# Optimization experiments

Hardware: AMD Instinct MI355X
Metric: run time of the kernel (lower is better)

## Reference

```python
import jax, jax.numpy as jnp
import numpy as np

B, L, D = 64, 1, 1024
H, HD = 16, 64          # num_heads, head_dim
T = 2048                # max kv-cache length
DFF = 4 * D
EPS = 1e-5


def _layernorm(x, w, b):
    mu = jnp.mean(x, axis=-1, keepdims=True)
    var = jnp.mean(jnp.square(x - mu), axis=-1, keepdims=True)
    return (x - mu) * jax.lax.rsqrt(var + EPS) * w + b


def setup_inputs() -> dict:
    key = jax.random.key(0)
    ks = jax.random.split(key, 12)
    s = 0.02
    x = jax.random.normal(ks[0], (B, L, D), jnp.float32)
    k_cache = jax.random.normal(ks[1], (B, H, T, HD), jnp.float32)
    v_cache = jax.random.normal(ks[2], (B, H, T, HD), jnp.float32)
    kv_cache_len = jax.random.randint(ks[3], (B,), 1024, T - 1)
    batch_indices = jnp.arange(B)
    # attend to all cache slots up to and including the newly written token
    attn_mask = (jnp.arange(T)[None, None, None, :] <= kv_cache_len[:, None, None, None])
    return {
        "x": x, "k_cache": k_cache, "v_cache": v_cache,
        "attn_mask": attn_mask, "kv_cache_len": kv_cache_len,
        "batch_indices": batch_indices,
        "qkv_w": jax.random.normal(ks[4], (D, 3 * D), jnp.float32) * s,
        "qkv_b": jnp.zeros((3 * D,), jnp.float32),
        "out_w": jax.random.normal(ks[5], (D, D), jnp.float32) * s,
        "out_b": jnp.zeros((D,), jnp.float32),
        "ln1_w": jnp.ones((D,), jnp.float32), "ln1_b": jnp.zeros((D,), jnp.float32),
        "ln2_w": jnp.ones((D,), jnp.float32), "ln2_b": jnp.zeros((D,), jnp.float32),
        "mlp_w1": jax.random.normal(ks[6], (D, DFF), jnp.float32) * s,
        "mlp_b1": jnp.zeros((DFF,), jnp.float32),
        "mlp_w2": jax.random.normal(ks[7], (DFF, D), jnp.float32) * s,
        "mlp_b2": jnp.zeros((D,), jnp.float32),
    }


def reference(x, k_cache, v_cache, attn_mask, kv_cache_len, batch_indices,
              qkv_w, qkv_b, out_w, out_b, ln1_w, ln1_b, ln2_w, ln2_b,
              mlp_w1, mlp_b1, mlp_w2, mlp_b2):
    b, l, d = x.shape
    residual = x
    qkv = (x @ qkv_w + qkv_b).reshape(b, l, 3, H, HD)
    q, k, v = qkv[:, :, 0], qkv[:, :, 1], qkv[:, :, 2]   # [B,L,H,HD]
    q = jnp.transpose(q, (0, 2, 1, 3))                    # [B,H,1,HD]
    k = jnp.transpose(k, (0, 2, 1, 3))
    v = jnp.transpose(v, (0, 2, 1, 3))
    # scatter new K/V into per-batch cache slot kv_cache_len
    k_cache = k_cache.at[batch_indices, :, kv_cache_len].set(k[:, :, 0])
    v_cache = v_cache.at[batch_indices, :, kv_cache_len].set(v[:, :, 0])
    # SDPA over full cache, single query token
    scores = jnp.einsum("bhqd,bhkd->bhqk", q, k_cache) * (1.0 / np.sqrt(HD))
    scores = jnp.where(attn_mask, scores, -jnp.inf)       # bool mask: True = attend
    attn = jax.nn.softmax(scores, axis=-1)
    o = jnp.einsum("bhqk,bhkd->bhqd", attn, v_cache)
    o = jnp.transpose(o, (0, 2, 1, 3)).reshape(b, l, d)
    x = residual + (o @ out_w + out_b)
    x = _layernorm(x, ln1_w, ln1_b)
    residual = x
    h = jax.nn.relu(x @ mlp_w1 + mlp_b1) @ mlp_w2 + mlp_b2
    x = _layernorm(residual + h, ln2_w, ln2_b)
    return x
```

## Files before the change

### kernel.cpp

```cpp
#include <hip/hip_runtime.h>
#include <hip/hip_bf16.h>
#include <math.h>

#define D_MODEL 1024
#define NH 16
#define HD 64
#define TMAX 2048
#define DFF 4096
#define NB 64
#define ACS 256
#define NC (TMAX / ACS)

template<int KC>
__global__ void gemm64_part(const float* __restrict__ X,
                            const float* __restrict__ W,
                            float* __restrict__ P,
                            int K, int N) {
    const int tx = threadIdx.x & 63;
    const int ty = threadIdx.x >> 6;
    const int n  = blockIdx.x * 64 + tx;
    const int k0 = blockIdx.y * KC;

    __shared__ float Xs[64][KC];

    for (int idx = threadIdx.x; idx < 64 * (KC / 4); idx += 256) {
        const int b  = idx / (KC / 4);
        const int kk = (idx % (KC / 4)) * 4;
        *reinterpret_cast<float4*>(&Xs[b][kk]) =
            *reinterpret_cast<const float4*>(&X[(size_t)b * K + k0 + kk]);
    }
    __syncthreads();

    float acc[16] = {0.f,0.f,0.f,0.f,0.f,0.f,0.f,0.f,
                     0.f,0.f,0.f,0.f,0.f,0.f,0.f,0.f};
    const float* Wp = W + (size_t)k0 * N + n;
#pragma unroll
    for (int kk = 0; kk < KC; kk += 4) {
        const float w0 = Wp[(size_t)(kk+0) * N];
        const float w1 = Wp[(size_t)(kk+1) * N];
        const float w2 = Wp[(size_t)(kk+2) * N];
        const float w3 = Wp[(size_t)(kk+3) * N];
#pragma unroll
        for (int i = 0; i < 16; ++i) {
            const float4 xv = *reinterpret_cast<const float4*>(&Xs[ty*16 + i][kk]);
            acc[i] += xv.x*w0 + xv.y*w1 + xv.z*w2 + xv.w*w3;
        }
    }

    float* Pp = P + (size_t)blockIdx.y * 64 * N + n;
#pragma unroll
    for (int i = 0; i < 16; ++i)
        Pp[(size_t)(ty*16 + i) * N] = acc[i];
}

template<bool RELU>
__global__ void reduce_kernel(const float* __restrict__ P,
                              const float* __restrict__ bias,
                              float* __restrict__ Y,
                              int N, int S) {
    const int i = blockIdx.x * 256 + threadIdx.x;
    const int n = i % N;
    float s = 0.0f;
    for (int ss = 0; ss < S; ++ss)
        s += P[(size_t)ss * 64 * N + i];
    s += bias[n];
    if (RELU)  s = fmaxf(s, 0.0f);
    Y[i] = s;
}

template<int S>
__global__ void reduce_ln_kernel(const float* __restrict__ P,
                                 const float* __restrict__ bias,
                                 const float* __restrict__ resid,
                                 const float* __restrict__ lnw,
                                 const float* __restrict__ lnb,
                                 float* __restrict__ Y) {
    const int b   = blockIdx.x;
    const int tid = threadIdx.x;
    float v[4];
    float s = 0.f, sq = 0.f;
#pragma unroll
    for (int jj = 0; jj < 4; ++jj) {
        const int n = jj * 256 + tid;
        float t = bias[n] + resid[(size_t)b * D_MODEL + n];
#pragma unroll
        for (int ss = 0; ss < S; ++ss)
            t += P[((size_t)ss * 64 + b) * D_MODEL + n];
        v[jj] = t; s += t; sq += t * t;
    }
    for (int off = 1; off < 64; off <<= 1) {
        s  += __shfl_xor(s, off);
        sq += __shfl_xor(sq, off);
    }
    __shared__ float rs[4], rq[4];
    const int wave = tid >> 6;
    if ((tid & 63) == 0) { rs[wave] = s; rq[wave] = sq; }
    __syncthreads();
    s  = rs[0] + rs[1] + rs[2] + rs[3];
    sq = rq[0] + rq[1] + rq[2] + rq[3];
    const float mean = s * (1.0f / D_MODEL);
    const float var  = sq * (1.0f / D_MODEL) - mean * mean;
    const float rstd = rsqrtf(var + 1e-5f);
#pragma unroll
    for (int jj = 0; jj < 4; ++jj) {
        const int n = jj * 256 + tid;
        Y[(size_t)b * D_MODEL + n] = (v[jj] - mean) * rstd * lnw[n] + lnb[n];
    }
}

__global__ void attn_part(const float* __restrict__ qkv,
                          const float* __restrict__ k_cache,
                          const float* __restrict__ v_cache,
                          const int* __restrict__ kv_len,
                          float* __restrict__ m_ws,
                          float* __restrict__ s_ws,
                          float* __restrict__ o_ws) {
    const int b = blockIdx.x;
    const int h = blockIdx.y;
    const int c = blockIdx.z;
    const int tid = threadIdx.x;

    const int L  = kv_len[b];
    const int nt = L + 1;
    const int c0 = c * ACS;
    if (c0 >= nt) return;
    const int tend = min(ACS, nt - c0);
    const bool full = (c0 + ACS <= L);

    __shared__ float q_s[HD];
    __shared__ float p_s[ACS];
    __shared__ float red[8];
    __shared__ float ored[16][HD + 4];

    const float* qkv_row = qkv + (size_t)b * (3 * D_MODEL);
    if (tid < HD) q_s[tid] = qkv_row[h * HD + tid] * 0.125f;
    __syncthreads();

    const size_t bh = ((size_t)b * NH + h) * (size_t)TMAX * HD;
    const float* kc   = k_cache + bh + (size_t)c0 * HD;
    const float* vc   = v_cache + bh + (size_t)c0 * HD;
    const float* knew = qkv_row + D_MODEL     + h * HD;
    const float* vnew = qkv_row + 2 * D_MODEL + h * HD;
    const int Lloc = L - c0;

    const int rg = tid >> 4, l16 = tid & 15;
    const float4 qf = *reinterpret_cast<const float4*>(&q_s[l16 * 4]);
    if (full) {
        float4 kf[16];
#pragma unroll
        for (int j = 0; j < 16; ++j)
            kf[j] = *reinterpret_cast<const float4*>(&kc[(size_t)(rg + j * 16) * HD + l16 * 4]);
#pragma unroll
        for (int j = 0; j < 16; ++j) {
            float d = qf.x*kf[j].x + qf.y*kf[j].y + qf.z*kf[j].z + qf.w*kf[j].w;
            d += __shfl_xor(d, 1);
            d += __shfl_xor(d, 2);
            d += __shfl_xor(d, 4);
            d += __shfl_xor(d, 8);
            if (l16 == 0) p_s[rg + j * 16] = d;
        }
    } else {
        for (int t = rg; t < tend; t += 16) {
            const float* krow = (t == Lloc) ? knew : (kc + (size_t)t * HD);
            const float4 kf = *reinterpret_cast<const float4*>(&krow[l16 * 4]);
            float d = qf.x*kf.x + qf.y*kf.y + qf.z*kf.z + qf.w*kf.w;
            d += __shfl_xor(d, 1);
            d += __shfl_xor(d, 2);
            d += __shfl_xor(d, 4);
            d += __shfl_xor(d, 8);
            if (l16 == 0) p_s[t] = d;
        }
    }

    const int d4 = tid & 15, r = tid >> 4;
    float4 vreg[16];
    if (full) {
#pragma unroll
        for (int j = 0; j < 16; ++j)
            vreg[j] = *reinterpret_cast<const float4*>(&vc[(size_t)(r + j * 16) * HD + d4 * 4]);
    } else {
#pragma unroll
        for (int j = 0; j < 16; ++j) {
            const int t = r + j * 16;
            if (t < tend) {
                const float* vrow = (t == Lloc) ? vnew : (vc + (size_t)t * HD);
                vreg[j] = *reinterpret_cast<const float4*>(&vrow[d4 * 4]);
            } else {
                vreg[j] = make_float4(0.f, 0.f, 0.f, 0.f);
            }
        }
    }
    __syncthreads();

    const float pv = (tid < tend) ? p_s[tid] : -INFINITY;
    float m = pv;
    for (int off = 1; off < 64; off <<= 1) m = fmaxf(m, __shfl_xor(m, off));
    const int wave = tid >> 6;
    if ((tid & 63) == 0) red[wave] = m;
    __syncthreads();
    m = fmaxf(fmaxf(red[0], red[1]), fmaxf(red[2], red[3]));

    float e = (tid < tend) ? expf(pv - m) : 0.0f;
    p_s[tid] = e;
    float s = e;
    for (int off = 1; off < 64; off <<= 1) s += __shfl_xor(s, off);
    if ((tid & 63) == 0) red[4 + wave] = s;
    __syncthreads();
    const float ssum = red[4] + red[5] + red[6] + red[7];

    float4 acc = make_float4(0.f, 0.f, 0.f, 0.f);
#pragma unroll
    for (int j = 0; j < 16; ++j) {
        const float p = p_s[r + j * 16];
        acc.x += p * vreg[j].x; acc.y += p * vreg[j].y;
        acc.z += p * vreg[j].z; acc.w += p * vreg[j].w;
    }
    *reinterpret_cast<float4*>(&ored[r][d4 * 4]) = acc;
    __syncthreads();

    const size_t idx = ((size_t)b * NH + h) * NC + c;
    if (tid == 0) { m_ws[idx] = m; s_ws[idx] = ssum; }
    if (tid < HD) {
        float o = 0.0f;
#pragma unroll
        for (int g = 0; g < 16; ++g) o += ored[g][tid];
        o_ws[idx * HD + tid] = o;
    }
}

__global__ void attn_combine(const float* __restrict__ m_ws,
                             const float* __restrict__ s_ws,
                             const float* __restrict__ o_ws,
                             const int* __restrict__ kv_len,
                             float* __restrict__ o) {
    const int b = blockIdx.x;
    const int h = blockIdx.y;
    const int d = threadIdx.x;
    const int nt = kv_len[b] + 1;
    const int nc = (nt + ACS - 1) / ACS;
    const size_t idx0 = ((size_t)b * NH + h) * NC;

    float M = -INFINITY;
    for (int c = 0; c < nc; ++c) M = fmaxf(M, m_ws[idx0 + c]);
    float den = 0.0f, num = 0.0f;
    for (int c = 0; c < nc; ++c) {
        const float w = expf(m_ws[idx0 + c] - M);
        den += w * s_ws[idx0 + c];
        num += w * o_ws[(idx0 + c) * HD + d];
    }
    o[(size_t)b * D_MODEL + h * HD + d] = num / den;
}

extern "C" void kernel_launch(void* const* d_in, const int* in_sizes, int n_in,
                              void* d_out, int out_size, void* d_ws, size_t ws_size,
                              hipStream_t stream) {
    const float* x       = (const float*)d_in[0];
    const float* k_cache = (const float*)d_in[1];
    const float* v_cache = (const float*)d_in[2];
    const int*   kv_len  = (const int*)d_in[4];
    const float* qkv_w   = (const float*)d_in[6];
    const float* qkv_b   = (const float*)d_in[7];
    const float* out_w   = (const float*)d_in[8];
    const float* out_b   = (const float*)d_in[9];
    const float* ln1_w   = (const float*)d_in[10];
    const float* ln1_b   = (const float*)d_in[11];
    const float* ln2_w   = (const float*)d_in[12];
    const float* ln2_b   = (const float*)d_in[13];
    const float* mlp_w1  = (const float*)d_in[14];
    const float* mlp_b1  = (const float*)d_in[15];
    const float* mlp_w2  = (const float*)d_in[16];
    const float* mlp_b2  = (const float*)d_in[17];

    float* out = (float*)d_out;
    float* ws  = (float*)d_ws;
    float* qkv = ws;
    float* o   = ws + 196608;
    float* t2  = ws + 262144;
    float* t3  = ws + 327680;
    float* P   = ws + 589824;
    float* m_ws = P;
    float* s_ws = P + 8192;
    float* o_ws = P + 16384;

    gemm64_part<64><<<dim3(48, 16), 256, 0, stream>>>(x, qkv_w, P, 1024, 3072);
    reduce_kernel<false><<<768, 256, 0, stream>>>(P, qkv_b, qkv, 3072, 16);

    attn_part<<<dim3(NB, NH, NC), 256, 0, stream>>>(qkv, k_cache, v_cache, kv_len, m_ws, s_ws, o_ws);
    attn_combine<<<dim3(NB, NH), 64, 0, stream>>>(m_ws, s_ws, o_ws, kv_len, o);

    gemm64_part<64><<<dim3(16, 16), 256, 0, stream>>>(o, out_w, P, 1024, 1024);
    reduce_ln_kernel<16><<<64, 256, 0, stream>>>(P, out_b, x, ln1_w, ln1_b, t2);

    gemm64_part<64><<<dim3(64, 16), 256, 0, stream>>>(t2, mlp_w1, P, 1024, 4096);
    reduce_kernel<true><<<1024, 256, 0, stream>>>(P, mlp_b1, t3, 4096, 16);

    gemm64_part<64><<<dim3(16, 64), 256, 0, stream>>>(t3, mlp_w2, P, 4096, 1024);
    reduce_ln_kernel<64><<<64, 256, 0, stream>>>(P, mlp_b2, t2, ln2_w, ln2_b, out);
}
```

Measured before the change: 275.4 us.

## Make each wave process an independent 64-token attention chunk without shared memory

The attention split kernel now gives each 64-lane wave its own 64-token chunk of the KV cache. Scores, softmax partials and the PV accumulation stay in registers and wave shuffles, so block-level shared memory and __syncthreads barriers are gone. The combine step now merges four times as many partial chunks, and the workspace offsets are enlarged to fit them. Waves past the sequence end still exit early, while the extra partial outputs add some combine work and workspace traffic.

```diff
diff --git a/kernel.cpp b/kernel.cpp
--- a/kernel.cpp
+++ b/kernel.cpp
@@ -8,8 +8,8 @@
 #define TMAX 2048
 #define DFF 4096
 #define NB 64
-#define ACS 256
-#define NC (TMAX / ACS)
+#define WCS 64
+#define NCW (TMAX / WCS)
 
 template<int KC>
 __global__ void gemm64_part(const float* __restrict__ X,
@@ -115,117 +115,81 @@
                           float* __restrict__ m_ws,
                           float* __restrict__ s_ws,
                           float* __restrict__ o_ws) {
-    const int b = blockIdx.x;
-    const int h = blockIdx.y;
-    const int c = blockIdx.z;
-    const int tid = threadIdx.x;
+    const int b    = blockIdx.x;
+    const int h    = blockIdx.y;
+    const int wave = threadIdx.x >> 6;
+    const int lane = threadIdx.x & 63;
+    const int cw   = blockIdx.z * 4 + wave;
 
     const int L  = kv_len[b];
     const int nt = L + 1;
-    const int c0 = c * ACS;
+    const int c0 = cw * WCS;
     if (c0 >= nt) return;
-    const int tend = min(ACS, nt - c0);
-    const bool full = (c0 + ACS <= L);
-
-    __shared__ float q_s[HD];
-    __shared__ float p_s[ACS];
-    __shared__ float red[8];
-    __shared__ float ored[16][HD + 4];
+    const int Lloc = L - c0;
+
+    const int rg = lane >> 4, l16 = lane & 15;
 
     const float* qkv_row = qkv + (size_t)b * (3 * D_MODEL);
-    if (tid < HD) q_s[tid] = qkv_row[h * HD + tid] * 0.125f;
-    __syncthreads();
-
-    const size_t bh = ((size_t)b * NH + h) * (size_t)TMAX * HD;
-    const float* kc   = k_cache + bh + (size_t)c0 * HD;
-    const float* vc   = v_cache + bh + (size_t)c0 * HD;
     const float* knew = qkv_row + D_MODEL     + h * HD;
     const float* vnew = qkv_row + 2 * D_MODEL + h * HD;
-    const int Lloc = L - c0;
-
-    const int rg = tid >> 4, l16 = tid & 15;
-    const float4 qf = *reinterpret_cast<const float4*>(&q_s[l16 * 4]);
-    if (full) {
-        float4 kf[16];
-#pragma unroll
-        for (int j = 0; j < 16; ++j)
-            kf[j] = *reinterpret_cast<const float4*>(&kc[(size_t)(rg + j * 16) * HD + l16 * 4]);
-#pragma unroll
-        for (int j = 0; j < 16; ++j) {
-            float d = qf.x*kf[j].x + qf.y*kf[j].y + qf.z*kf[j].z + qf.w*kf[j].w;
-            d += __shfl_xor(d, 1);
-            d += __shfl_xor(d, 2);
-            d += __shfl_xor(d, 4);
-            d += __shfl_xor(d, 8);
-            if (l16 == 0) p_s[rg + j * 16] = d;
-        }
-    } else {
-        for (int t = rg; t < tend; t += 16) {
-            const float* krow = (t == Lloc) ? knew : (kc + (size_t)t * HD);
-            const float4 kf = *reinterpret_cast<const float4*>(&krow[l16 * 4]);
-            float d = qf.x*kf.x + qf.y*kf.y + qf.z*kf.z + qf.w*kf.w;
-            d += __shfl_xor(d, 1);
-            d += __shfl_xor(d, 2);
-            d += __shfl_xor(d, 4);
-            d += __shfl_xor(d, 8);
-            if (l16 == 0) p_s[t] = d;
-        }
-    }
-
-    const int d4 = tid & 15, r = tid >> 4;
-    float4 vreg[16];
-    if (full) {
-#pragma unroll
-        for (int j = 0; j < 16; ++j)
-            vreg[j] = *reinterpret_cast<const float4*>(&vc[(size_t)(r + j * 16) * HD + d4 * 4]);
-    } else {
-#pragma unroll
-        for (int j = 0; j < 16; ++j) {
-            const int t = r + j * 16;
-            if (t < tend) {
-                const float* vrow = (t == Lloc) ? vnew : (vc + (size_t)t * HD);
-                vreg[j] = *reinterpret_cast<const float4*>(&vrow[d4 * 4]);
-            } else {
-                vreg[j] = make_float4(0.f, 0.f, 0.f, 0.f);
-            }
-        }
-    }
-    __syncthreads();
-
-    const float pv = (tid < tend) ? p_s[tid] : -INFINITY;
-    float m = pv;
-    for (int off = 1; off < 64; off <<= 1) m = fmaxf(m, __shfl_xor(m, off));
-    const int wave = tid >> 6;
-    if ((tid & 63) == 0) red[wave] = m;
-    __syncthreads();
-    m = fmaxf(fmaxf(red[0], red[1]), fmaxf(red[2], red[3]));
-
-    float e = (tid < tend) ? expf(pv - m) : 0.0f;
-    p_s[tid] = e;
-    float s = e;
-    for (int off = 1; off < 64; off <<= 1) s += __shfl_xor(s, off);
-    if ((tid & 63) == 0) red[4 + wave] = s;
-    __syncthreads();
-    const float ssum = red[4] + red[5] + red[6] + red[7];
+
+    float4 qf = *reinterpret_cast<const float4*>(&qkv_row[h * HD + l16 * 4]);
+    qf.x *= 0.125f; qf.y *= 0.125f; qf.z *= 0.125f; qf.w *= 0.125f;
+
+    const size_t bh = ((size_t)b * NH + h) * (size_t)TMAX * HD;
+    const float* kc = k_cache + bh + (size_t)c0 * HD;
+    const float* vc = v_cache + bh + (size_t)c0 * HD;
+
+    float d[16];
+#pragma unroll
+    for (int j = 0; j < 16; ++j) {
+        const int t = 4 * j + rg;
+        const float* krow = (t == Lloc) ? &knew[l16 * 4]
+                                        : &kc[(size_t)t * HD + l16 * 4];
+        const float4 kf = *reinterpret_cast<const float4*>(krow);
+        float sc = qf.x*kf.x + qf.y*kf.y + qf.z*kf.z + qf.w*kf.w;
+        sc += __shfl_xor(sc, 1);
+        sc += __shfl_xor(sc, 2);
+        sc += __shfl_xor(sc, 4);
+        sc += __shfl_xor(sc, 8);
+        d[j] = (t <= Lloc) ? sc : -INFINITY;
+    }
+
+    float m = d[0];
+#pragma unroll
+    for (int j = 1; j < 16; ++j) m = fmaxf(m, d[j]);
+    m = fmaxf(m, __shfl_xor(m, 16));
+    m = fmaxf(m, __shfl_xor(m, 32));
+
+    float e[16];
+    float s = 0.0f;
+#pragma unroll
+    for (int j = 0; j < 16; ++j) {
+        e[j] = expf(d[j] - m);
+        s += e[j];
+    }
+    s += __shfl_xor(s, 16);
+    s += __shfl_xor(s, 32);
 
     float4 acc = make_float4(0.f, 0.f, 0.f, 0.f);
 #pragma unroll
     for (int j = 0; j < 16; ++j) {
-        const float p = p_s[r + j * 16];
-        acc.x += p * vreg[j].x; acc.y += p * vreg[j].y;
-        acc.z += p * vreg[j].z; acc.w += p * vreg[j].w;
-    }
-    *reinterpret_cast<float4*>(&ored[r][d4 * 4]) = acc;
-    __syncthreads();
-
-    const size_t idx = ((size_t)b * NH + h) * NC + c;
-    if (tid == 0) { m_ws[idx] = m; s_ws[idx] = ssum; }
-    if (tid < HD) {
-        float o = 0.0f;
-#pragma unroll
-        for (int g = 0; g < 16; ++g) o += ored[g][tid];
-        o_ws[idx * HD + tid] = o;
-    }
+        const int t = 4 * j + rg;
+        const float* vrow = (t == Lloc) ? &vnew[l16 * 4]
+                                        : &vc[(size_t)t * HD + l16 * 4];
+        const float4 vv = *reinterpret_cast<const float4*>(vrow);
+        acc.x += e[j] * vv.x; acc.y += e[j] * vv.y;
+        acc.z += e[j] * vv.z; acc.w += e[j] * vv.w;
+    }
+    acc.x += __shfl_xor(acc.x, 16); acc.y += __shfl_xor(acc.y, 16);
+    acc.z += __shfl_xor(acc.z, 16); acc.w += __shfl_xor(acc.w, 16);
+    acc.x += __shfl_xor(acc.x, 32); acc.y += __shfl_xor(acc.y, 32);
+    acc.z += __shfl_xor(acc.z, 32); acc.w += __shfl_xor(acc.w, 32);
+
+    const size_t idx = ((size_t)b * NH + h) * NCW + cw;
+    if (lane == 0) { m_ws[idx] = m; s_ws[idx] = s; }
+    if (rg == 0)
+        *reinterpret_cast<float4*>(&o_ws[idx * HD + l16 * 4]) = acc;
 }
 
 __global__ void attn_combine(const float* __restrict__ m_ws,
@@ -237,8 +201,8 @@
     const int h = blockIdx.y;
     const int d = threadIdx.x;
     const int nt = kv_len[b] + 1;
-    const int nc = (nt + ACS - 1) / ACS;
-    const size_t idx0 = ((size_t)b * NH + h) * NC;
+    const int nc = (nt + WCS - 1) / WCS;
+    const size_t idx0 = ((size_t)b * NH + h) * NCW;
 
     float M = -INFINITY;
     for (int c = 0; c < nc; ++c) M = fmaxf(M, m_ws[idx0 + c]);
@@ -279,13 +243,13 @@
     float* t3  = ws + 327680;
     float* P   = ws + 589824;
     float* m_ws = P;
-    float* s_ws = P + 8192;
-    float* o_ws = P + 16384;
+    float* s_ws = P + 32768;
+    float* o_ws = P + 65536;
 
     gemm64_part<64><<<dim3(48, 16), 256, 0, stream>>>(x, qkv_w, P, 1024, 3072);
     reduce_kernel<false><<<768, 256, 0, stream>>>(P, qkv_b, qkv, 3072, 16);
 
-    attn_part<<<dim3(NB, NH, NC), 256, 0, stream>>>(qkv, k_cache, v_cache, kv_len, m_ws, s_ws, o_ws);
+    attn_part<<<dim3(NB, NH, NCW / 4), 256, 0, stream>>>(qkv, k_cache, v_cache, kv_len, m_ws, s_ws, o_ws);
     attn_combine<<<dim3(NB, NH), 64, 0, stream>>>(m_ws, s_ws, o_ws, kv_len, o);
 
     gemm64_part<64><<<dim3(16, 16), 256, 0, stream>>>(o, out_w, P, 1024, 1024);
```

New measurement: 291.3 us. 5.8% more time.
